# Kernel tuning notes

Measured on AMD Instinct MI355X. Metric: run time of the kernel, lower is better.

Reference implementation:

```python
import jax, jax.numpy as jnp
import numpy as np

INHIBITION = 3.0

def kwta(x, gates):
    # per-row k = argmax index of the gate row; keep the top-k values of x,
    # damp all other entries by 1/INHIBITION (matches torch loop + topk + scatter)
    k = jnp.argmax(gates, axis=1)                          # [B] int
    ranks = jnp.argsort(jnp.argsort(-x, axis=1), axis=1)   # rank 0 == largest
    keep = ranks < k[:, None]
    return jnp.where(keep, x, x / INHIBITION)

def _linear_init(key, out_d, in_d):
    k1, k2 = jax.random.split(key)
    lim = 1.0 / np.sqrt(in_d)
    W = jax.random.uniform(k1, (out_d, in_d), jnp.float32, -lim, lim)
    b = jax.random.uniform(k2, (out_d,), jnp.float32, -lim, lim)
    return W, b

def setup_inputs() -> dict:
    key = jax.random.key(0)
    B, S, H, HID = 16384, 512, 256, 512
    inp_dim = 2 * S + 4 + H  # 1284
    keys = jax.random.split(key, 13)
    d = {}
    d["state"] = jax.random.normal(keys[0], (B, 2 * S), jnp.float32)
    d["task_indicator"] = jax.random.normal(keys[1], (B, 4), jnp.float32)
    d["action"] = jax.random.normal(keys[2], (B, H), jnp.float32)
    specs = [("cx1_1", 2 * HID, inp_dim), ("cx1_2", 2 * HID, 2 * HID),
             ("cx2_1", HID, inp_dim), ("cx2_2", HID, HID),
             ("cx3_1", H, inp_dim), ("cx3_2", H, H),
             ("l1", 2 * HID, inp_dim), ("l2", HID, 2 * HID),
             ("l3", H, HID), ("l4", H, H)]
    for i, (name, o, idim) in enumerate(specs):
        W, b = _linear_init(keys[3 + i], o, idim)
        d["W_" + name] = W
        d["b_" + name] = b
    return d

def reference(state, task_indicator, action,
              W_cx1_1, b_cx1_1, W_cx1_2, b_cx1_2,
              W_cx2_1, b_cx2_1, W_cx2_2, b_cx2_2,
              W_cx3_1, b_cx3_1, W_cx3_2, b_cx3_2,
              W_l1, b_l1, W_l2, b_l2, W_l3, b_l3, W_l4, b_l4):
    ctx = jnp.concatenate([state, task_indicator, action], axis=1)  # [B, 1284]

    def gate(Wa, ba, Wb, bb):
        h = jnp.tanh(ctx @ Wa.T + ba)
        return jax.nn.softmax(h @ Wb.T + bb, axis=1)

    cx1 = gate(W_cx1_1, b_cx1_1, W_cx1_2, b_cx1_2)  # [B, 1024]
    cx2 = gate(W_cx2_1, b_cx2_1, W_cx2_2, b_cx2_2)  # [B, 512]
    cx3 = gate(W_cx3_1, b_cx3_1, W_cx3_2, b_cx3_2)  # [B, 256]

    x = kwta(ctx @ W_l1.T + b_l1, cx1)
    x = kwta(x @ W_l2.T + b_l2, cx2)
    x = kwta(x @ W_l3.T + b_l3, cx3)
    return x @ W_l4.T + b_l4  # [B, 256]
```

## Files before the change

kernel.cpp:

```cpp
#include <hip/hip_runtime.h>
#include <math.h>

typedef float  v4f   __attribute__((ext_vector_type(4)));
typedef double v2d   __attribute__((ext_vector_type(2)));
typedef double v4d   __attribute__((ext_vector_type(4)));
typedef float  f32x4 __attribute__((ext_vector_type(4)));
typedef short  s16x8 __attribute__((ext_vector_type(8)));

#define NB   16384
#define KCTX 1284
#define CSL  (KCTX/4)

#if defined(__has_builtin)
#  if __has_builtin(__builtin_amdgcn_mfma_f64_16x16x4f64)
#    define MFMA64(a, b, c) __builtin_amdgcn_mfma_f64_16x16x4f64((a), (b), (c), 0, 0, 0)
#  endif
#endif
#ifndef MFMA64
static __device__ __forceinline__ v4d mfma64_asm(double a, double b, v4d c) {
  asm volatile("v_mfma_f64_16x16x4_f64 %0, %1, %2, %0" : "+v"(c) : "v"(a), "v"(b));
  return c;
}
#  define MFMA64(a, b, c) mfma64_asm((a), (b), (c))
#endif

static __device__ __forceinline__ f32x4 mfma_bf16(s16x8 a, s16x8 b, f32x4 c) {
  asm("v_mfma_f32_16x16x32_bf16 %0, %1, %2, %0" : "+v"(c) : "v"(a), "v"(b));
  return c;
}

__global__ __launch_bounds__(256) void k_build_ctx(
    const float* __restrict__ state, const float* __restrict__ task,
    const float* __restrict__ action, float* __restrict__ Cg)
{
  int idx = blockIdx.x * 256 + threadIdx.x;
  if (idx >= NB * CSL) return;
  int b = idx / CSL, s = idx - b * CSL;
  v4f v;
  if (s < 256)       v = *((const v4f*)state  + (size_t)b * 256 + s);
  else if (s == 256) v = *((const v4f*)task   + b);
  else               v = *((const v4f*)action + (size_t)b * 64 + (s - 257));
  *((v4f*)Cg + idx) = v;
}

__device__ __forceinline__ unsigned long long f64_ord(double f) {
  unsigned long long u = (unsigned long long)__double_as_longlong(f);
  return (u & 0x8000000000000000ull) ? ~u : (u | 0x8000000000000000ull);
}

#define TM 128
#define TN 64
#define TK 16
#define LRA 130
#define LRB 66

template<int EPI, int ASRC>
__global__ __launch_bounds__(256, 3) void g64m(
    const void* __restrict__ Av, const float* __restrict__ W,
    const float* __restrict__ bias, void* __restrict__ Cv,
    unsigned long long* __restrict__ kpk, int N, int K)
{
  __shared__ __align__(16) double As[TK * LRA];
  __shared__ __align__(16) double Ws[TK * LRB];

  const int tid  = threadIdx.x;
  const int lane = tid & 63;
  const int wid  = tid >> 6;
  const int wm   = wid >> 1;
  const int wn   = wid & 1;
  const int grp  = lane >> 4;
  const int lid  = lane & 15;
  const int row0 = blockIdx.x * TM;
  const int col0 = blockIdx.y * TN;

  const int lrA = tid >> 1;
  const int lcA = (tid & 1) * 8;
  const int lrW = tid >> 2;
  const int lcW = (tid & 3) * 4;

  const float*  ApF = (const float*)Av  + (size_t)(row0 + lrA) * K;
  const double* ApD = (const double*)Av + (size_t)(row0 + lrA) * K;
  const float*  WpF = W + (size_t)(col0 + lrW) * K;

  double sa[8], sw[4];

  v4d acc[4][2];
  #pragma unroll
  for (int i = 0; i < 4; ++i)
    #pragma unroll
    for (int j = 0; j < 2; ++j) { acc[i][j][0] = 0.0; acc[i][j][1] = 0.0;
                                  acc[i][j][2] = 0.0; acc[i][j][3] = 0.0; }

  const int nt = (K + TK - 1) / TK;

  auto loadA = [&](int k0) {
    const int kb = k0 + lcA;
    if (ASRC == 0) {
      if (kb + 8 <= K) {
        v4f x0 = *(const v4f*)(ApF + kb), x1 = *(const v4f*)(ApF + kb + 4);
        sa[0] = x0.x; sa[1] = x0.y; sa[2] = x0.z; sa[3] = x0.w;
        sa[4] = x1.x; sa[5] = x1.y; sa[6] = x1.z; sa[7] = x1.w;
      } else {
        #pragma unroll
        for (int j = 0; j < 8; ++j) sa[j] = (kb + j < K) ? (double)ApF[kb + j] : 0.0;
      }
    } else {
      const double* p = ApD + kb;
      v2d d0 = *(const v2d*)p,       d1 = *(const v2d*)(p + 2);
      v2d d2 = *(const v2d*)(p + 4), d3 = *(const v2d*)(p + 6);
      sa[0] = d0.x; sa[1] = d0.y; sa[2] = d1.x; sa[3] = d1.y;
      sa[4] = d2.x; sa[5] = d2.y; sa[6] = d3.x; sa[7] = d3.y;
    }
  };
  auto loadW = [&](int k0) {
    const int kb = k0 + lcW;
    if (kb + 4 <= K) {
      v4f w0 = *(const v4f*)(WpF + kb);
      sw[0] = w0.x; sw[1] = w0.y; sw[2] = w0.z; sw[3] = w0.w;
    } else {
      #pragma unroll
      for (int j = 0; j < 4; ++j) sw[j] = (kb + j < K) ? (double)WpF[kb + j] : 0.0;
    }
  };

  loadA(0); loadW(0);

  for (int t = 0; t < nt; ++t) {
    __syncthreads();
    #pragma unroll
    for (int j = 0; j < 8; ++j) As[(lcA + j) * LRA + lrA] = sa[j];
    #pragma unroll
    for (int j = 0; j < 4; ++j) Ws[(lcW + j) * LRB + lrW] = sw[j];
    if (t + 1 < nt) { loadA((t + 1) * TK); loadW((t + 1) * TK); }
    __syncthreads();
    #pragma unroll
    for (int ks = 0; ks < 4; ++ks) {
      const double* Ar = As + (ks * 4 + grp) * LRA + wm * 64 + lid;
      const double* Br = Ws + (ks * 4 + grp) * LRB + wn * 32 + lid;
      double a[4], b[2];
      #pragma unroll
      for (int i = 0; i < 4; ++i) a[i] = Ar[i * 16];
      #pragma unroll
      for (int j = 0; j < 2; ++j) b[j] = Br[j * 16];
      #pragma unroll
      for (int i = 0; i < 4; ++i)
        #pragma unroll
        for (int j = 0; j < 2; ++j)
          acc[i][j] = MFMA64(a[i], b[j], acc[i][j]);
    }
  }

  double bb[2];
  #pragma unroll
  for (int j = 0; j < 2; ++j) bb[j] = (double)bias[col0 + wn * 32 + j * 16 + lid];

  if (EPI == 0) {
    #pragma unroll
    for (int i = 0; i < 4; ++i)
      #pragma unroll
      for (int r = 0; r < 4; ++r) {
        int row = row0 + wm * 64 + i * 16 + r * 4 + grp;
        double* Cp = (double*)Cv + (size_t)row * N + col0 + wn * 32 + lid;
        #pragma unroll
        for (int j = 0; j < 2; ++j) Cp[j * 16] = acc[i][j][r] + bb[j];
      }
  } else if (EPI == 3 || EPI == 4) {
    #pragma unroll
    for (int i = 0; i < 4; ++i)
      #pragma unroll
      for (int r = 0; r < 4; ++r) {
        int row = row0 + wm * 64 + i * 16 + r * 4 + grp;
        float* Cp = (float*)Cv + (size_t)row * N + col0 + wn * 32 + lid;
        #pragma unroll
        for (int j = 0; j < 2; ++j) {
          double o = acc[i][j][r] + bb[j];
          if (EPI == 4) o = tanh(o);
          Cp[j * 16] = (float)o;
        }
      }
  } else {
    #pragma unroll
    for (int i = 0; i < 4; ++i)
      #pragma unroll
      for (int r = 0; r < 4; ++r) {
        int row = row0 + wm * 64 + i * 16 + r * 4 + grp;
        double best = acc[i][0][r] + bb[0];
        int bcol = col0 + wn * 32 + lid;
        {
          double v = acc[i][1][r] + bb[1];
          if (v > best) { best = v; bcol = col0 + wn * 32 + 16 + lid; }
        }
        #pragma unroll
        for (int d = 1; d < 16; d <<= 1) {
          double ov = __shfl_xor(best, d);
          int    oc = __shfl_xor(bcol, d);
          if (ov > best || (ov == best && oc < bcol)) { best = ov; bcol = oc; }
        }
        if (lid == 0) {
          unsigned long long key =
              (f64_ord(best) & ~0xFFFFull) | ((~(unsigned)bcol) & 0xFFFFu);
          atomicMax(&kpk[row], key);
        }
      }
  }
}

#define GTM 128
#define GTN 64
#define GTK 32
#define GLR 40

template<int EPI>
__global__ __launch_bounds__(256, 2) void g16(
    const float* __restrict__ A, const float* __restrict__ W,
    const float* __restrict__ bias, float* __restrict__ C,
    unsigned long long* __restrict__ kpk, int N, int K)
{
  __shared__ __align__(16) unsigned short Al[3][GTM * GLR];
  __shared__ __align__(16) unsigned short Wl[3][GTN * GLR];

  const int tid  = threadIdx.x;
  const int lane = tid & 63;
  const int wid  = tid >> 6;
  const int wm   = wid >> 1;
  const int wn   = wid & 1;
  const int grp  = lane >> 4;
  const int lid  = lane & 15;
  const int row0 = blockIdx.x * GTM;
  const int col0 = blockIdx.y * GTN;

  const int arow = tid >> 1, akc = (tid & 1) * 16;
  const int wrow = tid >> 2, wkc = (tid & 3) * 8;
  const float* Ap = A + (size_t)(row0 + arow) * K;
  const float* Wp = W + (size_t)(col0 + wrow) * K;

  float av[16], wv[8];

  f32x4 ah[4][2], am[4][2], al[4][2];
  double sh[4][2][4];
  #pragma unroll
  for (int i = 0; i < 4; ++i)
    #pragma unroll
    for (int j = 0; j < 2; ++j) {
      ah[i][j] = (f32x4)0.f; am[i][j] = (f32x4)0.f; al[i][j] = (f32x4)0.f;
      #pragma unroll
      for (int r = 0; r < 4; ++r) sh[i][j][r] = 0.0;
    }

  const int nt = (K + GTK - 1) / GTK;

  auto loadA = [&](int kb) {
    #pragma unroll
    for (int q = 0; q < 4; ++q) {
      int k = kb + akc + q * 4;
      if (k + 4 <= K) {
        v4f x = *(const v4f*)(Ap + k);
        av[q*4+0] = x.x; av[q*4+1] = x.y; av[q*4+2] = x.z; av[q*4+3] = x.w;
      } else {
        #pragma unroll
        for (int j = 0; j < 4; ++j) av[q*4+j] = (k + j < K) ? Ap[k + j] : 0.f;
      }
    }
  };
  auto loadW = [&](int kb) {
    #pragma unroll
    for (int q = 0; q < 2; ++q) {
      int k = kb + wkc + q * 4;
      if (k + 4 <= K) {
        v4f x = *(const v4f*)(Wp + k);
        wv[q*4+0] = x.x; wv[q*4+1] = x.y; wv[q*4+2] = x.z; wv[q*4+3] = x.w;
      } else {
        #pragma unroll
        for (int j = 0; j < 4; ++j) wv[q*4+j] = (k + j < K) ? Wp[k + j] : 0.f;
      }
    }
  };

  auto split8 = [](const float* v, s16x8& p1, s16x8& p2, s16x8& p3) {
    #pragma unroll
    for (int j = 0; j < 8; ++j) {
      unsigned u1 = __float_as_uint(v[j]);
      float f1 = __uint_as_float(u1 & 0xFFFF0000u);
      float r1 = v[j] - f1;
      unsigned u2 = __float_as_uint(r1);
      float f2 = __uint_as_float(u2 & 0xFFFF0000u);
      float r2 = r1 - f2;
      unsigned u3 = __float_as_uint(r2);
      p1[j] = (short)(u1 >> 16); p2[j] = (short)(u2 >> 16); p3[j] = (short)(u3 >> 16);
    }
  };

  loadA(0); loadW(0);

  for (int t = 0; t < nt; ++t) {
    __syncthreads();
    #pragma unroll
    for (int h = 0; h < 2; ++h) {
      s16x8 p1, p2, p3;
      split8(&av[h * 8], p1, p2, p3);
      *(s16x8*)&Al[0][arow * GLR + akc + h * 8] = p1;
      *(s16x8*)&Al[1][arow * GLR + akc + h * 8] = p2;
      *(s16x8*)&Al[2][arow * GLR + akc + h * 8] = p3;
    }
    {
      s16x8 q1, q2, q3;
      split8(&wv[0], q1, q2, q3);
      *(s16x8*)&Wl[0][wrow * GLR + wkc] = q1;
      *(s16x8*)&Wl[1][wrow * GLR + wkc] = q2;
      *(s16x8*)&Wl[2][wrow * GLR + wkc] = q3;
    }
    if (t + 1 < nt) { loadA((t + 1) * GTK); loadW((t + 1) * GTK); }
    __syncthreads();

    s16x8 b0[2], b1[2], b2[2];
    #pragma unroll
    for (int nf = 0; nf < 2; ++nf) {
      int widx = (wn * 32 + nf * 16 + lid) * GLR + grp * 8;
      b0[nf] = *(const s16x8*)&Wl[0][widx];
      b1[nf] = *(const s16x8*)&Wl[1][widx];
      b2[nf] = *(const s16x8*)&Wl[2][widx];
    }
    #pragma unroll
    for (int mf = 0; mf < 4; ++mf) {
      int aidx = (wm * 64 + mf * 16 + lid) * GLR + grp * 8;
      s16x8 a0 = *(const s16x8*)&Al[0][aidx];
      s16x8 a1 = *(const s16x8*)&Al[1][aidx];
      s16x8 a2 = *(const s16x8*)&Al[2][aidx];
      #pragma unroll
      for (int nf = 0; nf < 2; ++nf) {
        ah[mf][nf] = mfma_bf16(a0, b0[nf], ah[mf][nf]);
        am[mf][nf] = mfma_bf16(a0, b1[nf], am[mf][nf]);
        am[mf][nf] = mfma_bf16(a1, b0[nf], am[mf][nf]);
        al[mf][nf] = mfma_bf16(a0, b2[nf], al[mf][nf]);
        al[mf][nf] = mfma_bf16(a1, b1[nf], al[mf][nf]);
        al[mf][nf] = mfma_bf16(a2, b0[nf], al[mf][nf]);
      }
    }
    if ((t & 7) == 7) {
      asm volatile("s_nop 7\n\ts_nop 7");
      #pragma unroll
      for (int mf = 0; mf < 4; ++mf)
        #pragma unroll
        for (int nf = 0; nf < 2; ++nf) {
          #pragma unroll
          for (int r = 0; r < 4; ++r) sh[mf][nf][r] += (double)ah[mf][nf][r];
          ah[mf][nf] = (f32x4)0.f;
        }
    }
  }

  asm volatile("s_nop 7\n\ts_nop 7");
  #pragma unroll
  for (int mf = 0; mf < 4; ++mf)
    #pragma unroll
    for (int nf = 0; nf < 2; ++nf)
      #pragma unroll
      for (int r = 0; r < 4; ++r) sh[mf][nf][r] += (double)ah[mf][nf][r];

  double bb[2];
  #pragma unroll
  for (int nf = 0; nf < 2; ++nf) bb[nf] = (double)bias[col0 + wn * 32 + nf * 16 + lid];

  if (EPI == 4) {
    #pragma unroll
    for (int mf = 0; mf < 4; ++mf)
      #pragma unroll
      for (int r = 0; r < 4; ++r) {
        int row = row0 + wm * 64 + mf * 16 + grp * 4 + r;
        float* Cp = C + (size_t)row * N + col0 + wn * 32 + lid;
        #pragma unroll
        for (int nf = 0; nf < 2; ++nf) {
          double o = sh[mf][nf][r] + (double)am[mf][nf][r] + (double)al[mf][nf][r] + bb[nf];
          Cp[nf * 16] = (float)tanh(o);
        }
      }
  } else {
    #pragma unroll
    for (int mf = 0; mf < 4; ++mf)
      #pragma unroll
      for (int r = 0; r < 4; ++r) {
        int row = row0 + wm * 64 + mf * 16 + grp * 4 + r;
        double v0 = sh[mf][0][r] + (double)am[mf][0][r] + (double)al[mf][0][r] + bb[0];
        double v1 = sh[mf][1][r] + (double)am[mf][1][r] + (double)al[mf][1][r] + bb[1];
        double best = v0; int bcol = col0 + wn * 32 + lid;
        if (v1 > best) { best = v1; bcol = col0 + wn * 32 + 16 + lid; }
        #pragma unroll
        for (int d = 1; d < 16; d <<= 1) {
          double ov = __shfl_xor(best, d);
          int    oc = __shfl_xor(bcol, d);
          if (ov > best || (ov == best && oc < bcol)) { best = ov; bcol = oc; }
        }
        if (lid == 0) {
          unsigned long long key =
              (f64_ord(best) & ~0xFFFFull) | ((~(unsigned)bcol) & 0xFFFFu);
          atomicMax(&kpk[row], key);
        }
      }
  }
}

__global__ __launch_bounds__(256) void k_kwta64(
    double* __restrict__ X, int N, const unsigned long long* __restrict__ kpk)
{
  const int row = blockIdx.x;
  const int tid = threadIdx.x;
  double* x = X + (size_t)row * N;
  __shared__ unsigned long long su[1024];
  __shared__ int hist[256];
  __shared__ int scan[256];
  __shared__ int s_bin, s_base, s_cnt;

  unsigned long long p = kpk[row];
  int k = (int)((~p) & 0xFFFFull);

  for (int j = tid; j < N; j += 256) su[j] = f64_ord(x[j]);
  __syncthreads();

  unsigned long long uth = 0xFFFFFFFFFFFFFFFFull;
  if (k > 0) {
    int t = N - k;
    unsigned long long prefix = 0;
    for (int shift = 56; shift >= 0; shift -= 8) {
      hist[tid] = 0;
      __syncthreads();
      unsigned long long pm =
          (shift == 56) ? 0ull : ~((1ull << (shift + 8)) - 1ull);
      for (int j = tid; j < N; j += 256) {
        unsigned long long u = su[j];
        if ((u & pm) == prefix) atomicAdd(&hist[(int)((u >> shift) & 255)], 1);
      }
      __syncthreads();
      int v = hist[tid];
      scan[tid] = v;
      __syncthreads();
      for (int d = 1; d < 256; d <<= 1) {
        int add = (tid >= d) ? scan[tid - d] : 0;
        __syncthreads();
        scan[tid] += add;
        __syncthreads();
      }
      int incl = scan[tid];
      int excl = incl - hist[tid];
      if (hist[tid] > 0 && t >= excl && t < incl) {
        s_bin = tid; s_base = excl; s_cnt = hist[tid];
      }
      __syncthreads();
      prefix |= ((unsigned long long)s_bin) << shift;
      t -= s_base;
      int cnt = s_cnt;
      __syncthreads();
      if (cnt == 1) break;
    }
    uth = prefix;
  }
  __syncthreads();
  for (int j = tid; j < N; j += 256) {
    if (su[j] < uth) x[j] = x[j] / 3.0;
  }
}

extern "C" void kernel_launch(void* const* d_in, const int* in_sizes, int n_in,
                              void* d_out, int out_size, void* d_ws, size_t ws_size,
                              hipStream_t stream)
{
  const float* state   = (const float*)d_in[0];
  const float* task    = (const float*)d_in[1];
  const float* action  = (const float*)d_in[2];
  const float* W_cx1_1 = (const float*)d_in[3];  const float* b_cx1_1 = (const float*)d_in[4];
  const float* W_cx1_2 = (const float*)d_in[5];  const float* b_cx1_2 = (const float*)d_in[6];
  const float* W_cx2_1 = (const float*)d_in[7];  const float* b_cx2_1 = (const float*)d_in[8];
  const float* W_cx2_2 = (const float*)d_in[9];  const float* b_cx2_2 = (const float*)d_in[10];
  const float* W_cx3_1 = (const float*)d_in[11]; const float* b_cx3_1 = (const float*)d_in[12];
  const float* W_cx3_2 = (const float*)d_in[13]; const float* b_cx3_2 = (const float*)d_in[14];
  const float* W_l1    = (const float*)d_in[15]; const float* b_l1    = (const float*)d_in[16];
  const float* W_l2    = (const float*)d_in[17]; const float* b_l2    = (const float*)d_in[18];
  const float* W_l3    = (const float*)d_in[19]; const float* b_l3    = (const float*)d_in[20];
  const float* W_l4    = (const float*)d_in[21]; const float* b_l4    = (const float*)d_in[22];

  char* wsb = (char*)d_ws;
  double* A1 = (double*)wsb;
  float*  Hf = (float*)wsb;
  double* A3 = (double*)wsb;
  float*  Cg = (float*)(wsb + 134217728ULL);
  double* A2 = (double*)(wsb + 134217728ULL);
  unsigned long long* kpk = (unsigned long long*)d_out;

  dim3 blk(256);

  k_build_ctx<<<(NB * CSL) / 256, blk, 0, stream>>>(state, task, action, Cg);
  (void)hipMemsetAsync(kpk, 0, (size_t)3 * NB * 8, stream);

  g16<4><<<dim3(NB/GTM, 1024/GTN), blk, 0, stream>>>(Cg, W_cx1_1, b_cx1_1, Hf, nullptr, 1024, KCTX);
  g16<2><<<dim3(NB/GTM, 1024/GTN), blk, 0, stream>>>(Hf, W_cx1_2, b_cx1_2, nullptr, kpk,        1024, 1024);
  g16<4><<<dim3(NB/GTM,  512/GTN), blk, 0, stream>>>(Cg, W_cx2_1, b_cx2_1, Hf, nullptr, 512, KCTX);
  g16<2><<<dim3(NB/GTM,  512/GTN), blk, 0, stream>>>(Hf, W_cx2_2, b_cx2_2, nullptr, kpk + NB,    512,  512);
  g16<4><<<dim3(NB/GTM,  256/GTN), blk, 0, stream>>>(Cg, W_cx3_1, b_cx3_1, Hf, nullptr, 256, KCTX);
  g16<2><<<dim3(NB/GTM,  256/GTN), blk, 0, stream>>>(Hf, W_cx3_2, b_cx3_2, nullptr, kpk + 2*NB,  256,  256);

  g64m<0,0><<<dim3(NB/TM, 1024/TN), blk, 0, stream>>>(Cg, W_l1, b_l1, A1, nullptr, 1024, KCTX);
  k_kwta64<<<NB, blk, 0, stream>>>(A1, 1024, kpk);
  g64m<0,1><<<dim3(NB/TM,  512/TN), blk, 0, stream>>>(A1, W_l2, b_l2, A2, nullptr,  512, 1024);
  k_kwta64<<<NB, blk, 0, stream>>>(A2,  512, kpk + NB);
  g64m<0,1><<<dim3(NB/TM,  256/TN), blk, 0, stream>>>(A2, W_l3, b_l3, A3, nullptr,  256,  512);
  k_kwta64<<<NB, blk, 0, stream>>>(A3,  256, kpk + 2*NB);
  g64m<3,1><<<dim3(NB/TM,  256/TN), blk, 0, stream>>>(A3, W_l4, b_l4, d_out, nullptr, 256, 256);
}
```

Before: 2.336 ms.

## Pre-split gate weights and hidden activations into bf16 planes outside GEMM loops

```diff
diff --git a/kernel.cpp b/kernel.cpp
--- a/kernel.cpp
+++ b/kernel.cpp
@@ -48,6 +48,26 @@
   return (u & 0x8000000000000000ull) ? ~u : (u | 0x8000000000000000ull);
 }
 
+__global__ __launch_bounds__(256) void k_split_w(
+    const float* __restrict__ W, unsigned short* __restrict__ out,
+    int N, int K, int KP)
+{
+  int idx = blockIdx.x * 256 + threadIdx.x;
+  size_t total = (size_t)N * KP;
+  if (idx >= (int)total) return;
+  int n = idx / KP, k = idx - n * KP;
+  float v = (k < K) ? W[(size_t)n * K + k] : 0.f;
+  unsigned u1 = __float_as_uint(v);
+  float f1 = __uint_as_float(u1 & 0xFFFF0000u);
+  float r1 = v - f1;
+  unsigned u2 = __float_as_uint(r1);
+  float f2 = __uint_as_float(u2 & 0xFFFF0000u);
+  float r2 = r1 - f2;
+  out[idx]             = (unsigned short)(u1 >> 16);
+  out[total + idx]     = (unsigned short)(u2 >> 16);
+  out[2 * total + idx] = (unsigned short)(__float_as_uint(r2) >> 16);
+}
+
 #define TM 128
 #define TN 64
 #define TK 16
@@ -210,11 +230,13 @@
 #define GTK 32
 #define GLR 40
 
-template<int EPI>
+template<int EPI, int ASPLIT>
 __global__ __launch_bounds__(256, 2) void g16(
-    const float* __restrict__ A, const float* __restrict__ W,
-    const float* __restrict__ bias, float* __restrict__ C,
-    unsigned long long* __restrict__ kpk, int N, int K)
+    const void* __restrict__ Av, size_t aplane,
+    const unsigned short* __restrict__ WS_,
+    const float* __restrict__ bias,
+    unsigned short* __restrict__ Hout, size_t hplane,
+    unsigned long long* __restrict__ kpk, int N, int K, int KP)
 {
   __shared__ __align__(16) unsigned short Al[3][GTM * GLR];
   __shared__ __align__(16) unsigned short Wl[3][GTN * GLR];
@@ -231,10 +253,13 @@
 
   const int arow = tid >> 1, akc = (tid & 1) * 16;
   const int wrow = tid >> 2, wkc = (tid & 3) * 8;
-  const float* Ap = A + (size_t)(row0 + arow) * K;
-  const float* Wp = W + (size_t)(col0 + wrow) * K;
-
-  float av[16], wv[8];
+  const float*          ApF = (const float*)Av + (size_t)(row0 + arow) * K;
+  const unsigned short* ApS = (const unsigned short*)Av + (size_t)(row0 + arow) * K;
+  const unsigned short* WpS = WS_ + (size_t)(col0 + wrow) * KP + wkc;
+  const size_t wplane = (size_t)N * KP;
+
+  float av[16];
+  s16x8 sA[3][2], sW[3];
 
   f32x4 ah[4][2], am[4][2], al[4][2];
   double sh[4][2][4];
@@ -247,33 +272,34 @@
       for (int r = 0; r < 4; ++r) sh[i][j][r] = 0.0;
     }
 
-  const int nt = (K + GTK - 1) / GTK;
+  const int nt = KP / GTK;
 
   auto loadA = [&](int kb) {
-    #pragma unroll
-    for (int q = 0; q < 4; ++q) {
-      int k = kb + akc + q * 4;
-      if (k + 4 <= K) {
-        v4f x = *(const v4f*)(Ap + k);
-        av[q*4+0] = x.x; av[q*4+1] = x.y; av[q*4+2] = x.z; av[q*4+3] = x.w;
-      } else {
-        #pragma unroll
-        for (int j = 0; j < 4; ++j) av[q*4+j] = (k + j < K) ? Ap[k + j] : 0.f;
+    if (ASPLIT == 0) {
+      #pragma unroll
+      for (int q = 0; q < 4; ++q) {
+        int k = kb + akc + q * 4;
+        if (k + 4 <= K) {
+          v4f x = *(const v4f*)(ApF + k);
+          av[q*4+0] = x.x; av[q*4+1] = x.y; av[q*4+2] = x.z; av[q*4+3] = x.w;
+        } else {
+          #pragma unroll
+          for (int j = 0; j < 4; ++j) av[q*4+j] = (k + j < K) ? ApF[k + j] : 0.f;
+        }
+      }
+    } else {
+      #pragma unroll
+      for (int p = 0; p < 3; ++p) {
+        const unsigned short* s = ApS + p * aplane + kb + akc;
+        sA[p][0] = *(const s16x8*)s;
+        sA[p][1] = *(const s16x8*)(s + 8);
       }
     }
   };
   auto loadW = [&](int kb) {
     #pragma unroll
-    for (int q = 0; q < 2; ++q) {
-      int k = kb + wkc + q * 4;
-      if (k + 4 <= K) {
-        v4f x = *(const v4f*)(Wp + k);
-        wv[q*4+0] = x.x; wv[q*4+1] = x.y; wv[q*4+2] = x.z; wv[q*4+3] = x.w;
-      } else {
-        #pragma unroll
-        for (int j = 0; j < 4; ++j) wv[q*4+j] = (k + j < K) ? Wp[k + j] : 0.f;
-      }
-    }
+    for (int p = 0; p < 3; ++p)
+      sW[p] = *(const s16x8*)(WpS + p * wplane + kb);
   };
 
   auto split8 = [](const float* v, s16x8& p1, s16x8& p2, s16x8& p3) {
@@ -285,8 +311,8 @@
       unsigned u2 = __float_as_uint(r1);
       float f2 = __uint_as_float(u2 & 0xFFFF0000u);
       float r2 = r1 - f2;
-      unsigned u3 = __float_as_uint(r2);
-      p1[j] = (short)(u1 >> 16); p2[j] = (short)(u2 >> 16); p3[j] = (short)(u3 >> 16);
+      p1[j] = (short)(u1 >> 16); p2[j] = (short)(u2 >> 16);
+      p3[j] = (short)(__float_as_uint(r2) >> 16);
     }
   };
 
@@ -294,21 +320,25 @@
 
   for (int t = 0; t < nt; ++t) {
     __syncthreads();
-    #pragma unroll
-    for (int h = 0; h < 2; ++h) {
-      s16x8 p1, p2, p3;
-      split8(&av[h * 8], p1, p2, p3);
-      *(s16x8*)&Al[0][arow * GLR + akc + h * 8] = p1;
-      *(s16x8*)&Al[1][arow * GLR + akc + h * 8] = p2;
-      *(s16x8*)&Al[2][arow * GLR + akc + h * 8] = p3;
-    }
-    {
-      s16x8 q1, q2, q3;
-      split8(&wv[0], q1, q2, q3);
-      *(s16x8*)&Wl[0][wrow * GLR + wkc] = q1;
-      *(s16x8*)&Wl[1][wrow * GLR + wkc] = q2;
-      *(s16x8*)&Wl[2][wrow * GLR + wkc] = q3;
-    }
+    if (ASPLIT == 0) {
+      #pragma unroll
+      for (int h = 0; h < 2; ++h) {
+        s16x8 p1, p2, p3;
+        split8(&av[h * 8], p1, p2, p3);
+        *(s16x8*)&Al[0][arow * GLR + akc + h * 8] = p1;
+        *(s16x8*)&Al[1][arow * GLR + akc + h * 8] = p2;
+        *(s16x8*)&Al[2][arow * GLR + akc + h * 8] = p3;
+      }
+    } else {
+      #pragma unroll
+      for (int p = 0; p < 3; ++p) {
+        *(s16x8*)&Al[p][arow * GLR + akc]     = sA[p][0];
+        *(s16x8*)&Al[p][arow * GLR + akc + 8] = sA[p][1];
+      }
+    }
+    #pragma unroll
+    for (int p = 0; p < 3; ++p)
+      *(s16x8*)&Wl[p][wrow * GLR + wkc] = sW[p];
     if (t + 1 < nt) { loadA((t + 1) * GTK); loadW((t + 1) * GTK); }
     __syncthreads();
 
@@ -367,11 +397,20 @@
       #pragma unroll
       for (int r = 0; r < 4; ++r) {
         int row = row0 + wm * 64 + mf * 16 + grp * 4 + r;
-        float* Cp = C + (size_t)row * N + col0 + wn * 32 + lid;
+        size_t base = (size_t)row * N + col0 + wn * 32 + lid;
         #pragma unroll
         for (int nf = 0; nf < 2; ++nf) {
           double o = sh[mf][nf][r] + (double)am[mf][nf][r] + (double)al[mf][nf][r] + bb[nf];
-          Cp[nf * 16] = (float)tanh(o);
+          float f = (float)tanh(o);
+          unsigned u1 = __float_as_uint(f);
+          float f1 = __uint_as_float(u1 & 0xFFFF0000u);
+          float r1 = f - f1;
+          unsigned u2 = __float_as_uint(r1);
+          float f2 = __uint_as_float(u2 & 0xFFFF0000u);
+          float r2 = r1 - f2;
+          Hout[base + nf * 16]              = (unsigned short)(u1 >> 16);
+          Hout[hplane + base + nf * 16]     = (unsigned short)(u2 >> 16);
+          Hout[2 * hplane + base + nf * 16] = (unsigned short)(__float_as_uint(r2) >> 16);
         }
       }
   } else {
@@ -479,23 +518,44 @@
 
   char* wsb = (char*)d_ws;
   double* A1 = (double*)wsb;
-  float*  Hf = (float*)wsb;
+  unsigned short* HfS = (unsigned short*)wsb;
   double* A3 = (double*)wsb;
+  unsigned short* WS  = (unsigned short*)(wsb + 100663296ULL);
   float*  Cg = (float*)(wsb + 134217728ULL);
   double* A2 = (double*)(wsb + 134217728ULL);
   unsigned long long* kpk = (unsigned long long*)d_out;
 
+  const size_t o_c11 = 0;
+  const size_t o_c12 = 4030464;
+  const size_t o_c21 = 7176192;
+  const size_t o_c22 = 9191424;
+  const size_t o_c31 = 9977856;
+  const size_t o_c32 = 10985472;
+
   dim3 blk(256);
 
   k_build_ctx<<<(NB * CSL) / 256, blk, 0, stream>>>(state, task, action, Cg);
   (void)hipMemsetAsync(kpk, 0, (size_t)3 * NB * 8, stream);
 
-  g16<4><<<dim3(NB/GTM, 1024/GTN), blk, 0, stream>>>(Cg, W_cx1_1, b_cx1_1, Hf, nullptr, 1024, KCTX);
-  g16<2><<<dim3(NB/GTM, 1024/GTN), blk, 0, stream>>>(Hf, W_cx1_2, b_cx1_2, nullptr, kpk,        1024, 1024);
-  g16<4><<<dim3(NB/GTM,  512/GTN), blk, 0, stream>>>(Cg, W_cx2_1, b_cx2_1, Hf, nullptr, 512, KCTX);
-  g16<2><<<dim3(NB/GTM,  512/GTN), blk, 0, stream>>>(Hf, W_cx2_2, b_cx2_2, nullptr, kpk + NB,    512,  512);
-  g16<4><<<dim3(NB/GTM,  256/GTN), blk, 0, stream>>>(Cg, W_cx3_1, b_cx3_1, Hf, nullptr, 256, KCTX);
-  g16<2><<<dim3(NB/GTM,  256/GTN), blk, 0, stream>>>(Hf, W_cx3_2, b_cx3_2, nullptr, kpk + 2*NB,  256,  256);
+  k_split_w<<<(1024*1312 + 255)/256, blk, 0, stream>>>(W_cx1_1, WS + o_c11, 1024, KCTX, 1312);
+  k_split_w<<<(1024*1024 + 255)/256, blk, 0, stream>>>(W_cx1_2, WS + o_c12, 1024, 1024, 1024);
+  k_split_w<<<( 512*1312 + 255)/256, blk, 0, stream>>>(W_cx2_1, WS + o_c21,  512, KCTX, 1312);
+  k_split_w<<<( 512* 512 + 255)/256, blk, 0, stream>>>(W_cx2_2, WS + o_c22,  512,  512,  512);
+  k_split_w<<<( 256*1312 + 255)/256, blk, 0, stream>>>(W_cx3_1, WS + o_c31,  256, KCTX, 1312);
+  k_split_w<<<( 256* 256 + 255)/256, blk, 0, stream>>>(W_cx3_2, WS + o_c32,  256,  256,  256);
+
+  g16<4,0><<<dim3(NB/GTM, 1024/GTN), blk, 0, stream>>>(Cg, 0, WS + o_c11, b_cx1_1,
+      HfS, (size_t)NB * 1024, nullptr, 1024, KCTX, 1312);
+  g16<2,1><<<dim3(NB/GTM, 1024/GTN), blk, 0, stream>>>(HfS, (size_t)NB * 1024, WS + o_c12, b_cx1_2,
+      nullptr, 0, kpk, 1024, 1024, 1024);
+  g16<4,0><<<dim3(NB/GTM,  512/GTN), blk, 0, stream>>>(Cg, 0, WS + o_c21, b_cx2_1,
+      HfS, (size_t)NB * 512, nullptr, 512, KCTX, 1312);
+  g16<2,1><<<dim3(NB/GTM,  512/GTN), blk, 0, stream>>>(HfS, (size_t)NB * 512, WS + o_c22, b_cx2_2,
+      nullptr, 0, kpk + NB, 512, 512, 512);
+  g16<4,0><<<dim3(NB/GTM,  256/GTN), blk, 0, stream>>>(Cg, 0, WS + o_c31, b_cx3_1,
+      HfS, (size_t)NB * 256, nullptr, 256, KCTX, 1312);
+  g16<2,1><<<dim3(NB/GTM,  256/GTN), blk, 0, stream>>>(HfS, (size_t)NB * 256, WS + o_c32, b_cx3_2,
+      nullptr, 0, kpk + 2 * NB, 256, 256, 256);
 
   g64m<0,0><<<dim3(NB/TM, 1024/TN), blk, 0, stream>>>(Cg, W_l1, b_l1, A1, nullptr, 1024, KCTX);
   k_kwta64<<<NB, blk, 0, stream>>>(A1, 1024, kpk);
```

New measurement: 2.353 ms. Within noise of the previous version (+0.7%).
